# Kernel tuning notes

Hardware: AMD Instinct MI355X
Metric: run time of the kernel (lower is better)

The kernel has to match this reference:

```python
import jax, jax.numpy as jnp
import numpy as np

B, C, T = 16, 256, 2048          # bsz, z_dim (fsz), tsz
PRED_STEPS, N_NEG, OFFSET = 12, 15, 16
COPIES = 1 + N_NEG


def setup_inputs() -> dict:
    key = jax.random.key(0)
    k1, k2, k3 = jax.random.split(key, 3)
    z = jax.random.normal(k1, (B, C, T), jnp.float32)
    # ConvTranspose2d(C, C, (1, PRED_STEPS)) weight, size-1 kernel-height dim dropped
    weight = jax.random.normal(k2, (C, C, PRED_STEPS), jnp.float32) * 0.02
    bias = jnp.zeros((C,), jnp.float32)
    # negative index sampling (done under no_grad in the original):
    # tszs[k] = k // N_NEG, r in [0, B*T-1), bump by 1 where r >= t
    tszs = jnp.repeat(jnp.arange(T, dtype=jnp.int32), N_NEG)   # (N_NEG*T,)
    r = jax.random.randint(k3, (B, N_NEG * T), 0, B * T - 1, dtype=jnp.int32)
    neg_idxs = r + (r >= tszs[None, :]).astype(jnp.int32)      # values in [0, B*T)
    return {"z": z, "weight": weight, "bias": bias, "neg_idxs": neg_idxs}


def reference(z, weight, bias, neg_idxs):
    # encoder / aggregator are identity: z_hat = z
    # predictor: pred_steps independent linear maps of z_hat
    z_pred = jnp.einsum('bct,coi->boti', z, weight) + bias[None, :, None, None]  # (B,C,T,S)

    # --- sample_negatives: gather from flattened (C, B*T) bank ---
    y = jnp.transpose(z, (1, 0, 2)).reshape(C, B * T)           # (C, B*T)
    negs = y[:, neg_idxs.reshape(-1)]                           # (C, B*N_NEG*T)
    negs = negs.reshape(C, B, N_NEG, T)
    negs = jnp.transpose(negs, (2, 1, 0, 3))                    # (N_NEG, B, C, T)

    targets = jnp.concatenate([z[None], negs], axis=0)          # (COPIES, B, C, T)

    steps = min(PRED_STEPS, T - OFFSET)
    preds = []
    for i in range(steps):  # fixed small structural loop (12 steps)
        off = i + OFFSET
        # ('bct,nbct->tbn') on the overlapping slices, written flat
        p = jnp.einsum('bct,nbct->tbn', z_pred[:, :, :T - off, i], targets[..., off:])
        preds.append(p.reshape(-1))
    predictions = jnp.concatenate(preds).reshape(-1, COPIES)
    labels = jnp.zeros((predictions.shape[0],), dtype=jnp.int32)
    return predictions, labels
```

## Files before the change

### kernel.cpp

```cpp
#include <hip/hip_runtime.h>
#include <hip/hip_bf16.h>

#define B_   16
#define C_   256
#define T_   2048
#define PS   12
#define NNEG 15
#define OFFS 16
#define COPIES 16

#define M_GEMM (B_ * T_)
#define N_GEMM (C_ * PS)
#define K_GEMM C_
#define NPRED 6225408
#define NLAB  389088

using bf16 = __hip_bfloat16;
typedef __attribute__((ext_vector_type(4))) float f32x4;
typedef __attribute__((ext_vector_type(8))) short bf16x8;

#define WAITVM(n) asm volatile("s_waitcnt vmcnt(" #n ")" ::: "memory")
#define GLL(src, dst)                                                        \
    __builtin_amdgcn_global_load_lds(                                        \
        (const __attribute__((address_space(1))) void*)(src),                \
        (__attribute__((address_space(3))) void*)(dst), 16, 0, 0)

__global__ __launch_bounds__(256) void transpose_z(const float* __restrict__ z,
                                                   bf16* __restrict__ zT) {
    __shared__ float tile[32][33];
    int t0 = blockIdx.x * 32, c0 = blockIdx.y * 32, b = blockIdx.z;
    int col = threadIdx.x & 31, r = threadIdx.x >> 5;
    for (int rr = 0; rr < 4; ++rr) {
        int row = r + rr * 8;
        tile[row][col] = z[(size_t)(b * C_ + c0 + row) * T_ + t0 + col];
    }
    __syncthreads();
    for (int rr = 0; rr < 4; ++rr) {
        int row = r + rr * 8;
        zT[(size_t)(b * T_ + t0 + row) * C_ + c0 + col] =
            __float2bfloat16(tile[col][row]);
    }
}

__global__ __launch_bounds__(256) void pack_w(const float* __restrict__ w,
                                              bf16* __restrict__ wTb) {
    int gid = blockIdx.x * 256 + threadIdx.x;
    int j = gid >> 8, c = gid & 255;
    int o = j & 255, i = j >> 8;
    wTb[gid] = __float2bfloat16(w[(size_t)c * (C_ * PS) + o * PS + i]);
}

#define EPAD 136

__global__ __launch_bounds__(256) void gemm_zpred(const bf16* __restrict__ zT,
                                                  const bf16* __restrict__ wTb,
                                                  const float* __restrict__ bias,
                                                  bf16* __restrict__ zp) {
    __shared__ __align__(16) char smem[49152];
    bf16* lE = (bf16*)smem;

    int bid = (blockIdx.x & 7) * 768 + (blockIdx.x >> 3);
    int bn = bid % (N_GEMM / 128);
    int bm = bid / (N_GEMM / 128);
    int tid = threadIdx.x;
    int wid = tid >> 6, lane = tid & 63;
    int ln15 = lane & 15, kg = lane >> 4;
    int wm = (wid & 1) * 64, wn = (wid >> 1) * 64;
    int row0 = bm * 128, col0 = bn * 128;
    int i_step = col0 >> 8;
    int o0 = col0 & 255;

    int gsw = ((lane & 3) ^ ((lane >> 3) & 3)) * 8;
    int srow = wid * 16 + (lane >> 2);
    const bf16* srcA = zT + (size_t)(row0 + srow) * 256 + gsw;
    const bf16* srcB = wTb + (size_t)(col0 + srow) * 256 + gsw;

    int offA[4], offB[4];
#pragma unroll
    for (int mi = 0; mi < 4; ++mi) {
        int r = wm + mi * 16 + ln15;
        offA[mi] = r * 64 + ((kg ^ ((r >> 1) & 3)) * 16);
    }
#pragma unroll
    for (int ni = 0; ni < 4; ++ni) {
        int c = wn + ni * 16 + ln15;
        offB[ni] = 8192 + c * 64 + ((kg ^ ((c >> 1) & 3)) * 16);
    }

    f32x4 acc[4][4] = {};

#define STAGE(t, slot_base)                                                  \
    {                                                                        \
        char* d = smem + (slot_base) + wid * 1024;                           \
        const bf16* sa = srcA + (t) * 32;                                    \
        const bf16* sb2 = srcB + (t) * 32;                                   \
        GLL(sa, d);                                                          \
        GLL(sa + 64 * 256, d + 4096);                                        \
        GLL(sb2, d + 8192);                                                  \
        GLL(sb2 + 64 * 256, d + 12288);                                      \
    }

#define TILE_BODY(slot_base, VMN)                                            \
    {                                                                        \
        WAITVM(VMN);                                                         \
        __builtin_amdgcn_s_barrier();                                        \
        const char* sb = smem + (slot_base);                                 \
        bf16x8 af[4], bfr[4];                                                \
        _Pragma("unroll") for (int mi = 0; mi < 4; ++mi)                     \
            af[mi] = *(const bf16x8*)(sb + offA[mi]);                        \
        _Pragma("unroll") for (int ni = 0; ni < 4; ++ni)                     \
            bfr[ni] = *(const bf16x8*)(sb + offB[ni]);                       \
        asm volatile("s_waitcnt lgkmcnt(0)" ::: "memory");                   \
        __builtin_amdgcn_sched_barrier(0);                                   \
        __builtin_amdgcn_s_barrier();                                        \
        __builtin_amdgcn_s_setprio(1);                                       \
        _Pragma("unroll") for (int mi = 0; mi < 4; ++mi)                     \
            _Pragma("unroll") for (int ni = 0; ni < 4; ++ni)                 \
                acc[mi][ni] = __builtin_amdgcn_mfma_f32_16x16x32_bf16(       \
                    af[mi], bfr[ni], acc[mi][ni], 0, 0, 0);                  \
        __builtin_amdgcn_s_setprio(0);                                       \
    }

    STAGE(0, 0);
    STAGE(1, 16384);
    STAGE(2, 32768);  TILE_BODY(0, 8);
    STAGE(3, 0);      TILE_BODY(16384, 8);
    STAGE(4, 16384);  TILE_BODY(32768, 8);
    STAGE(5, 32768);  TILE_BODY(0, 8);
    STAGE(6, 0);      TILE_BODY(16384, 8);
    STAGE(7, 16384);  TILE_BODY(32768, 8);
                      TILE_BODY(0, 4);
                      TILE_BODY(16384, 0);

    __syncthreads();

    float bv[4];
#pragma unroll
    for (int ni = 0; ni < 4; ++ni) bv[ni] = bias[o0 + wn + ni * 16 + ln15];

#pragma unroll
    for (int mi = 0; mi < 4; ++mi)
#pragma unroll
        for (int ni = 0; ni < 4; ++ni) {
            int col_e = wn + ni * 16 + ln15;
#pragma unroll
            for (int r = 0; r < 4; ++r) {
                int row_e = wm + mi * 16 + kg * 4 + r;
                lE[row_e * EPAD + col_e] = __float2bfloat16(acc[mi][ni][r] + bv[ni]);
            }
        }

    __syncthreads();

#pragma unroll
    for (int e = 0; e < 8; ++e) {
        int row_e = e * 16 + (tid >> 4);
        int grow = row0 + row_e;
        int b = grow >> 11, t = grow & (T_ - 1);
        int s = t + OFFS + i_step;
        if (s < T_) {
            bf16x8 v = *(const bf16x8*)&lE[row_e * EPAD + (tid & 15) * 8];
            *(bf16x8*)(zp + ((size_t)(b * T_ + s) * PS + i_step) * 256 + o0 +
                       (tid & 15) * 8) = v;
        }
    }
#undef STAGE
#undef TILE_BODY
}

__global__ __launch_bounds__(256) void predict_kernel(
    const bf16* __restrict__ zT, const bf16* __restrict__ zp,
    const int* __restrict__ neg, float* __restrict__ out) {
    int tid = threadIdx.x;
    int wid = tid >> 6, lane = tid & 63;
    int ln15 = lane & 15, kg = lane >> 4;
    int gw = (blockIdx.x * 4 + wid) * 2;
    int b = gw / (T_ - OFFS);
    int s = OFFS + gw % (T_ - OFFS);

    int src0, src1;
    if (ln15 == 0) {
        src0 = b * T_ + s;
        src1 = src0 + 1;
    } else {
        const int* np = neg + b * (NNEG * T_) + (ln15 - 1) * T_ + s;
        src0 = np[0];
        src1 = np[1];
    }
    const bf16* a0 = zT + (size_t)src0 * 256 + kg * 8;
    const bf16* a1 = zT + (size_t)src1 * 256 + kg * 8;
    const bf16* b0 = zp + ((size_t)(b * T_ + s) * PS + ln15) * 256 + kg * 8;
    const bf16* b1 = b0 + PS * 256;

    f32x4 acc0 = {0.f, 0.f, 0.f, 0.f};
    f32x4 acc1 = {0.f, 0.f, 0.f, 0.f};
#pragma unroll
    for (int kk = 0; kk < 8; ++kk) {
        bf16x8 av0 = *(const bf16x8*)(a0 + kk * 32);
        bf16x8 bv0 = *(const bf16x8*)(b0 + kk * 32);
        bf16x8 av1 = *(const bf16x8*)(a1 + kk * 32);
        bf16x8 bv1 = *(const bf16x8*)(b1 + kk * 32);
        acc0 = __builtin_amdgcn_mfma_f32_16x16x32_bf16(av0, bv0, acc0, 0, 0, 0);
        acc1 = __builtin_amdgcn_mfma_f32_16x16x32_bf16(av1, bv1, acc1, 0, 0, 0);
    }

    int i = ln15;
    if (i < PS) {
#pragma unroll 2
        for (int p = 0; p < 2; ++p) {
            int sp = s + p;
            int imax = sp - OFFS;
            if (i <= imax) {
                int t = sp - OFFS - i;
                int base_i = 256 * ((T_ - OFFS) * i - (i * (i - 1)) / 2);
                float* o = out + base_i + (t * B_ + b) * COPIES + kg * 4;
                f32x4 a = p ? acc1 : acc0;
                o[0] = a[0]; o[1] = a[1]; o[2] = a[2]; o[3] = a[3];
            }
        }
    }
}

extern "C" void kernel_launch(void* const* d_in, const int* in_sizes, int n_in,
                              void* d_out, int out_size, void* d_ws, size_t ws_size,
                              hipStream_t stream) {
    const float* z    = (const float*)d_in[0];
    const float* w    = (const float*)d_in[1];
    const float* bias = (const float*)d_in[2];
    const int*   neg  = (const int*)d_in[3];
    float* out = (float*)d_out;

    char* ws = (char*)d_ws;
    const size_t ZP_BYTES = (size_t)B_ * T_ * PS * 256 * sizeof(bf16);
    bf16* zp  = (bf16*)ws;
    bf16* zT  = (bf16*)(ws + ZP_BYTES + 8192);
    bf16* wTb = (bf16*)(ws + ZP_BYTES + 8192 + (size_t)M_GEMM * 256 * sizeof(bf16));

    transpose_z<<<dim3(T_ / 32, C_ / 32, B_), 256, 0, stream>>>(z, zT);
    pack_w<<<(N_GEMM * 256) / 256, 256, 0, stream>>>(w, wTb);
    gemm_zpred<<<(M_GEMM / 128) * (N_GEMM / 128), 256, 0, stream>>>(zT, wTb, bias, zp);
    predict_kernel<<<(B_ * (T_ - OFFS)) / 8, 256, 0, stream>>>(zT, zp, neg, out);
    hipMemsetAsync(out + NPRED, 0, NLAB * sizeof(float), stream);
}
```

Before: 159.9 us.

## Pipeline predict kernel with double-buffered async global-to-LDS loads per wave

Rewrites the predict kernel so each wave handles 8 consecutive (b,s) positions, staging the gathered z rows and z_pred rows into a swizzled LDS double buffer via global_load_lds. The next-but-one position is prefetched while the current one computes, so gather latency is meant to overlap with MFMA work and stores. The kernel now uses 128KB of shared memory per block, which limits occupancy to one block per CU, and launches 4x fewer blocks. Each iteration computes one position per MFMA chain instead of two interleaved ones.

```diff
diff --git a/kernel.cpp b/kernel.cpp
--- a/kernel.cpp
+++ b/kernel.cpp
@@ -171,53 +171,86 @@
 __global__ __launch_bounds__(256) void predict_kernel(
     const bf16* __restrict__ zT, const bf16* __restrict__ zp,
     const int* __restrict__ neg, float* __restrict__ out) {
+    __shared__ __align__(16) char psm[131072];
     int tid = threadIdx.x;
     int wid = tid >> 6, lane = tid & 63;
     int ln15 = lane & 15, kg = lane >> 4;
-    int gw = (blockIdx.x * 4 + wid) * 2;
-    int b = gw / (T_ - OFFS);
-    int s = OFFS + gw % (T_ - OFFS);
-
-    int src0, src1;
-    if (ln15 == 0) {
-        src0 = b * T_ + s;
-        src1 = src0 + 1;
-    } else {
-        const int* np = neg + b * (NNEG * T_) + (ln15 - 1) * T_ + s;
-        src0 = np[0];
-        src1 = np[1];
-    }
-    const bf16* a0 = zT + (size_t)src0 * 256 + kg * 8;
-    const bf16* a1 = zT + (size_t)src1 * 256 + kg * 8;
-    const bf16* b0 = zp + ((size_t)(b * T_ + s) * PS + ln15) * 256 + kg * 8;
-    const bf16* b1 = b0 + PS * 256;
-
-    f32x4 acc0 = {0.f, 0.f, 0.f, 0.f};
-    f32x4 acc1 = {0.f, 0.f, 0.f, 0.f};
-#pragma unroll
-    for (int kk = 0; kk < 8; ++kk) {
-        bf16x8 av0 = *(const bf16x8*)(a0 + kk * 32);
-        bf16x8 bv0 = *(const bf16x8*)(b0 + kk * 32);
-        bf16x8 av1 = *(const bf16x8*)(a1 + kk * 32);
-        bf16x8 bv1 = *(const bf16x8*)(b1 + kk * 32);
-        acc0 = __builtin_amdgcn_mfma_f32_16x16x32_bf16(av0, bv0, acc0, 0, 0, 0);
-        acc1 = __builtin_amdgcn_mfma_f32_16x16x32_bf16(av1, bv1, acc1, 0, 0, 0);
-    }
-
-    int i = ln15;
-    if (i < PS) {
-#pragma unroll 2
-        for (int p = 0; p < 2; ++p) {
-            int sp = s + p;
-            int imax = sp - OFFS;
-            if (i <= imax) {
-                int t = sp - OFFS - i;
-                int base_i = 256 * ((T_ - OFFS) * i - (i * (i - 1)) / 2);
-                float* o = out + base_i + (t * B_ + b) * COPIES + kg * 4;
-                f32x4 a = p ? acc1 : acc0;
-                o[0] = a[0]; o[1] = a[1]; o[2] = a[2]; o[3] = a[3];
-            }
-        }
+    char* my = psm + wid * 32768;
+    int base_gi = (blockIdx.x * 4 + wid) * 8;
+
+    const char* zTb = (const char*)zT;
+    const char* zpb = (const char*)zp;
+
+    auto stage = [&](int it, int slot) {
+        int gi = base_gi + it;
+        int b = gi / (T_ - OFFS);
+        int s = OFFS + gi % (T_ - OFFS);
+        int srcrow = 0;
+        if (lane < 16) {
+            if (lane == 0) srcrow = b * T_ + s;
+            else srcrow = neg[b * (NNEG * T_) + (lane - 1) * T_ + s];
+        }
+        char* dst = my + slot * 16384;
+        int half = lane >> 5;
+        int g31 = lane & 31;
+#pragma unroll
+        for (int j = 0; j < 8; ++j) {
+            int r0 = __shfl(srcrow, 2 * j);
+            int r1 = __shfl(srcrow, 2 * j + 1);
+            int row = half ? r1 : r0;
+            int n = 2 * j + half;
+            const char* src = zTb + (size_t)row * 512 + ((g31 ^ (n & 7)) << 4);
+            GLL(src, dst + j * 1024);
+        }
+        size_t zoff = (size_t)(b * T_ + s) * (PS * 512);
+#pragma unroll
+        for (int j = 0; j < 6; ++j) {
+            int i0 = 2 * j + half;
+            const char* src = zpb + zoff + i0 * 512 + ((g31 ^ (i0 & 7)) << 4);
+            GLL(src, dst + 8192 + j * 1024);
+        }
+    };
+
+    auto compute = [&](int it, int slot) {
+        const char* sb = my + slot * 16384;
+        int ii = ln15 < 12 ? ln15 : 0;
+        bf16x8 af[8], bfr[8];
+#pragma unroll
+        for (int kk = 0; kk < 8; ++kk) {
+            int g = kk * 4 + kg;
+            af[kk] = *(const bf16x8*)(sb + ln15 * 512 + ((g ^ (ln15 & 7)) << 4));
+            bfr[kk] = *(const bf16x8*)(sb + 8192 + ii * 512 + ((g ^ (ii & 7)) << 4));
+        }
+        asm volatile("s_waitcnt lgkmcnt(0)" ::: "memory");
+        __builtin_amdgcn_sched_barrier(0);
+        if (it + 2 < 8) stage(it + 2, slot);
+
+        f32x4 acc = {0.f, 0.f, 0.f, 0.f};
+#pragma unroll
+        for (int kk = 0; kk < 8; ++kk)
+            acc = __builtin_amdgcn_mfma_f32_16x16x32_bf16(af[kk], bfr[kk], acc,
+                                                          0, 0, 0);
+
+        int gi = base_gi + it;
+        int b = gi / (T_ - OFFS);
+        int s = OFFS + gi % (T_ - OFFS);
+        int i = ln15;
+        int imax = s - OFFS; if (imax > PS - 1) imax = PS - 1;
+        if (i <= imax) {
+            int t = s - OFFS - i;
+            int base_i = 256 * ((T_ - OFFS) * i - (i * (i - 1)) / 2);
+            float* o = out + base_i + (t * B_ + b) * COPIES + kg * 4;
+            o[0] = acc[0]; o[1] = acc[1]; o[2] = acc[2]; o[3] = acc[3];
+        }
+    };
+
+    stage(0, 0);
+    stage(1, 1);
+#pragma unroll
+    for (int it = 0; it < 8; ++it) {
+        if (it < 7) { WAITVM(14); }
+        else        { WAITVM(0);  }
+        compute(it, it & 1);
     }
 }
 
@@ -239,6 +272,6 @@
     transpose_z<<<dim3(T_ / 32, C_ / 32, B_), 256, 0, stream>>>(z, zT);
     pack_w<<<(N_GEMM * 256) / 256, 256, 0, stream>>>(w, wTb);
     gemm_zpred<<<(M_GEMM / 128) * (N_GEMM / 128), 256, 0, stream>>>(zT, wTb, bias, zp);
-    predict_kernel<<<(B_ * (T_ - OFFS)) / 8, 256, 0, stream>>>(zT, zp, neg, out);
+    predict_kernel<<<(B_ * (T_ - OFFS)) / 32, 256, 0, stream>>>(zT, zp, neg, out);
     hipMemsetAsync(out + NPRED, 0, NLAB * sizeof(float), stream);
 }
```

After: 152.0 us. 1.05x faster.
